# Optimization experiments

Hardware: AMD Instinct MI355X
Metric: run time of the kernel (lower is better)

Reference implementation:

```python
import jax, jax.numpy as jnp
import numpy as np

EPS = 1e-09

def setup_inputs() -> dict:
    key = jax.random.key(0)
    k1, k2, k3 = jax.random.split(key, 3)
    B, C, H, W = 16, 512, 64, 64
    K = 64  # node_num
    x = jax.random.normal(k1, (B, C, H, W), dtype=jnp.float32)
    anchor = jax.random.uniform(k2, (K, C), dtype=jnp.float32)
    sigma_raw = jax.random.uniform(k3, (K, C), dtype=jnp.float32)
    return {"x": x, "anchor": anchor, "sigma_raw": sigma_raw}

def _l2norm(v, axis):
    return v / jnp.maximum(jnp.linalg.norm(v, axis=axis, keepdims=True), 1e-12)

def reference(x, anchor, sigma_raw):
    B, C, H, W = x.shape
    K = anchor.shape[0]
    N = H * W
    sigma = jax.nn.sigmoid(sigma_raw)               # [K, C]
    xf = x.reshape(B, C, N).transpose(0, 2, 1)      # [B, N, C] descriptors

    # squared Mahalanobis-like distance ||(x - a_k)/s_k||^2 via expansion
    # (avoids materializing the [B, N, K, C] residual the torch loop builds)
    inv_s2 = 1.0 / (sigma * sigma)                  # [K, C]
    a_s2 = anchor * inv_s2                          # [K, C]
    const = jnp.sum(anchor * a_s2, axis=1)          # [K]
    d2 = (jnp.einsum('bnc,kc->bnk', xf * xf, inv_s2)
          - 2.0 * jnp.einsum('bnc,kc->bnk', xf, a_s2)
          + const[None, None, :])                   # [B, N, K]
    logits = (-0.5 * d2).transpose(0, 2, 1)         # [B, K, N]
    soft_assign = jax.nn.softmax(logits, axis=1)    # softmax over nodes

    # aggregation: nodes[b,k,c] = sum_n w * (x - a_k)/s_k / (sum_n w + eps)
    w_sum = jnp.sum(soft_assign, axis=2)            # [B, K]
    wx = jnp.einsum('bkn,bnc->bkc', soft_assign, xf)  # [B, K, C]
    nodes = (wx - w_sum[:, :, None] * anchor[None]) / sigma[None]
    nodes = nodes / (w_sum[:, :, None] + EPS)       # [B, K, C]

    nodes = _l2norm(nodes, axis=2)                  # intra-normalize per node
    flat = _l2norm(nodes.reshape(B, -1), axis=1)    # global L2
    # faithful to torch: flat [B, K*C] reinterpreted (no transpose) as [B, C, K]
    return flat.reshape(B, C, K), soft_assign
```

## Files before the change

### kernel.cpp

```cpp
#include <hip/hip_runtime.h>
#include <math.h>

#define B_ 16
#define C_ 512
#define N_ 4096
#define K_ 64

#define OFF_PBIG    0
#define OFF_INVSIG  131072
#define OFF_WSUM    163840
#define OFF_GSUM    164864
#define OFF_WX      164992

typedef short bf16x8 __attribute__((ext_vector_type(8)));
typedef float f32x16 __attribute__((ext_vector_type(16)));

union U4 { uint4 u; bf16x8 b; };

__device__ __forceinline__ unsigned hi16(float f) { return __float_as_uint(f) >> 16; }
__device__ __forceinline__ unsigned hi16rne(float f) {
  return (__float_as_uint(f) + 0x8000u) >> 16;
}
__device__ __forceinline__ float fromhi(unsigned h) { return __uint_as_float(h << 16); }
__device__ __forceinline__ unsigned pk(float lo, float hi) {
  return (__float_as_uint(lo) >> 16) | (__float_as_uint(hi) & 0xFFFF0000u);
}

__global__ void k_prep(const float* __restrict__ anchor,
                       const float* __restrict__ sraw,
                       unsigned* __restrict__ pbig,
                       float* __restrict__ invsig,
                       float* __restrict__ wsum,
                       float* __restrict__ gsum) {
  const int k = blockIdx.x;
  const int t = threadIdx.x;
  __shared__ float s_is2[C_], s_m[C_];
  __shared__ float red[4];
  float part = 0.f;
#pragma unroll
  for (int r = 0; r < 2; r++) {
    int c = r * 256 + t;
    float a = anchor[k * C_ + c];
    float sg = 1.f / (1.f + __expf(-sraw[k * C_ + c]));
    float is = 1.f / sg;
    float is2 = is * is;
    s_is2[c] = is2;
    s_m[c] = -2.f * a * is2;
    invsig[k * C_ + c] = is;
    part = fmaf(a * a, is2, part);
  }
  float v = part;
#pragma unroll
  for (int off = 32; off; off >>= 1) v += __shfl_down(v, off);
  if ((t & 63) == 0) red[t >> 6] = v;
  __syncthreads();
  float cst = red[0] + red[1] + red[2] + red[3];
  unsigned ch = hi16(cst);
  unsigned clr = hi16rne(cst - fromhi(ch));
#pragma unroll
  for (int r = 0; r < 2; r++) {
    int c = r * 256 + t;
    float is2 = s_is2[c], m = s_m[c];
    unsigned ih = hi16(is2);
    unsigned ilr = hi16rne(is2 - fromhi(ih));
    unsigned mh = hi16(m);
    unsigned mlr = hi16rne(m - fromhi(mh));
    unsigned* p = pbig + (size_t)k * 2048 + c * 4;
    p[0] = ih | (ilr << 16);
    p[1] = ih | (mh << 16);
    p[2] = mlr | (mh << 16);
    p[3] = (c == 0) ? (ch | (clr << 16)) : 0u;
  }
  if (k == 0) {
    for (int i = t; i < B_ * K_; i += 256) wsum[i] = 0.f;
    if (t < B_) gsum[t] = 0.f;
  }
}

__global__ __launch_bounds__(256) void k_dist(
    const float* __restrict__ x,
    const unsigned* __restrict__ pbig,
    float* __restrict__ soft,
    float* __restrict__ wsum) {
  const int b = blockIdx.y;
  const int nblk = blockIdx.x * 256;
  const int tid = threadIdx.x;
  const int wid = tid >> 6;
  const int lane = tid & 63;
  const int l31 = lane & 31;
  const int lh = lane >> 5;
  const int n0 = nblk + wid * 64;

  __shared__ unsigned ldsA[64 * 132];

  f32x16 acc[2][2];
#pragma unroll
  for (int kt = 0; kt < 2; kt++)
#pragma unroll
    for (int ns = 0; ns < 2; ns++)
#pragma unroll
      for (int i = 0; i < 16; i++) acc[kt][ns][i] = 0.f;

  const float* xb = x + (size_t)b * (C_ * N_);

  for (int chunk = 0; chunk < 16; chunk++) {
    const uint4* src = (const uint4*)pbig;
#pragma unroll
    for (int it = 0; it < 8; it++) {
      int flat = tid + it * 256;
      int k = flat >> 5, q = flat & 31;
      uint4 vv = src[(size_t)k * 512 + chunk * 32 + q];
      *(uint4*)&ldsA[k * 132 + q * 4] = vv;
    }
    __syncthreads();
    const int cchunk = chunk * 32;
    for (int kstep = 0; kstep < 16; kstep++) {
      U4 a0, a1;
      a0.u = *(const uint4*)&ldsA[l31 * 132 + kstep * 8 + lh * 4];
      a1.u = *(const uint4*)&ldsA[(32 + l31) * 132 + kstep * 8 + lh * 4];
      const int c = cchunk + kstep * 2 + lh;
      const float* xr = xb + (size_t)c * N_;
#pragma unroll
      for (int ns = 0; ns < 2; ns++) {
        float xv = xr[n0 + ns * 32 + l31];
        float x2 = xv * xv;
        unsigned u = __float_as_uint(xv);
        unsigned u2 = __float_as_uint(x2);
        unsigned uhf = u & 0xFFFF0000u;
        unsigned u2hf = u2 & 0xFFFF0000u;
        float xl = xv - __uint_as_float(uhf);
        float x2l = x2 - __uint_as_float(u2hf);
        U4 bf;
        bf.u.x = (u2 >> 16) | u2hf;
        bf.u.y = ((__float_as_uint(x2l) + 0x8000u) >> 16) | uhf;
        bf.u.z = (u >> 16) | ((__float_as_uint(xl) + 0x8000u) & 0xFFFF0000u);
        bf.u.w = (c == 0) ? 0x3F803F80u : 0u;
        acc[0][ns] = __builtin_amdgcn_mfma_f32_32x32x16_bf16(a0.b, bf.b, acc[0][ns], 0, 0, 0);
        acc[1][ns] = __builtin_amdgcn_mfma_f32_32x32x16_bf16(a1.b, bf.b, acc[1][ns], 0, 0, 0);
      }
    }
    __syncthreads();
  }

  float* softb = soft + (size_t)b * (K_ * N_);
#pragma unroll
  for (int ns = 0; ns < 2; ns++) {
    float mm = -3.4e38f;
#pragma unroll
    for (int kt = 0; kt < 2; kt++)
#pragma unroll
      for (int r = 0; r < 16; r++) {
        float l = -0.5f * acc[kt][ns][r];
        acc[kt][ns][r] = l;
        mm = fmaxf(mm, l);
      }
    mm = fmaxf(mm, __shfl_xor(mm, 32));
    float ss = 0.f;
#pragma unroll
    for (int kt = 0; kt < 2; kt++)
#pragma unroll
      for (int r = 0; r < 16; r++) {
        float e = __expf(acc[kt][ns][r] - mm);
        acc[kt][ns][r] = e;
        ss += e;
      }
    ss += __shfl_xor(ss, 32);
    float inv = 1.f / ss;
    const int nc = n0 + ns * 32 + l31;
#pragma unroll
    for (int kt = 0; kt < 2; kt++)
#pragma unroll
      for (int r = 0; r < 16; r++) {
        float w = acc[kt][ns][r] * inv;
        acc[kt][ns][r] = w;
        int k = kt * 32 + (r & 3) + 8 * (r >> 2) + 4 * lh;
        softb[(size_t)k * N_ + nc] = w;
      }
  }
#pragma unroll
  for (int kt = 0; kt < 2; kt++)
#pragma unroll
    for (int r = 0; r < 16; r++) {
      float v = acc[kt][0][r] + acc[kt][1][r];
      v += __shfl_xor(v, 1);
      v += __shfl_xor(v, 2);
      v += __shfl_xor(v, 4);
      v += __shfl_xor(v, 8);
      v += __shfl_xor(v, 16);
      if (l31 == 0) {
        int k = kt * 32 + (r & 3) + 8 * (r >> 2) + 4 * lh;
        atomicAdd(&wsum[b * K_ + k], v);
      }
    }
}

__global__ __launch_bounds__(256) void k_agg(const float* __restrict__ x,
                                             const float* __restrict__ soft,
                                             float* __restrict__ wx) {
  const int ct = blockIdx.x;
  const int b = blockIdx.y;
  const int tid = threadIdx.x;
  const int wid = tid >> 6, lane = tid & 63, l31 = lane & 31, lh = lane >> 5;
  const int c0 = ct * 32;
  const int n0 = wid * 1024;
  __shared__ float red[4][64][36];

  f32x16 acc[2];
#pragma unroll
  for (int kt = 0; kt < 2; kt++)
#pragma unroll
    for (int i = 0; i < 16; i++) acc[kt][i] = 0.f;

  const float* sb = soft + (size_t)b * (K_ * N_);
  const float* xr = x + (size_t)b * (C_ * N_) + (size_t)(c0 + l31) * N_;
  const float* s0 = sb + (size_t)l31 * N_;
  const float* s1 = sb + (size_t)(32 + l31) * N_;

  for (int kstep = 0; kstep < 64; kstep++) {
    int nb = n0 + kstep * 16 + lh * 8;
    float4 f0 = *(const float4*)&s0[nb];
    float4 f1 = *(const float4*)&s0[nb + 4];
    float4 g0 = *(const float4*)&s1[nb];
    float4 g1 = *(const float4*)&s1[nb + 4];
    float4 h0 = *(const float4*)&xr[nb];
    float4 h1 = *(const float4*)&xr[nb + 4];
    U4 A0, A1, Bf;
    A0.u.x = pk(f0.x, f0.y); A0.u.y = pk(f0.z, f0.w);
    A0.u.z = pk(f1.x, f1.y); A0.u.w = pk(f1.z, f1.w);
    A1.u.x = pk(g0.x, g0.y); A1.u.y = pk(g0.z, g0.w);
    A1.u.z = pk(g1.x, g1.y); A1.u.w = pk(g1.z, g1.w);
    Bf.u.x = pk(h0.x, h0.y); Bf.u.y = pk(h0.z, h0.w);
    Bf.u.z = pk(h1.x, h1.y); Bf.u.w = pk(h1.z, h1.w);
    acc[0] = __builtin_amdgcn_mfma_f32_32x32x16_bf16(A0.b, Bf.b, acc[0], 0, 0, 0);
    acc[1] = __builtin_amdgcn_mfma_f32_32x32x16_bf16(A1.b, Bf.b, acc[1], 0, 0, 0);
  }
#pragma unroll
  for (int kt = 0; kt < 2; kt++)
#pragma unroll
    for (int q = 0; q < 4; q++) {
      float4 vv = make_float4(acc[kt][q * 4], acc[kt][q * 4 + 1],
                              acc[kt][q * 4 + 2], acc[kt][q * 4 + 3]);
      *(float4*)&red[wid][lane][kt * 16 + q * 4] = vv;
    }
  __syncthreads();
  const int lt = tid & 63, sb4 = (tid >> 6) * 8;
  float v[8];
#pragma unroll
  for (int i = 0; i < 8; i++) v[i] = 0.f;
#pragma unroll
  for (int w = 0; w < 4; w++)
#pragma unroll
    for (int i = 0; i < 8; i++) v[i] += red[w][lt][sb4 + i];
#pragma unroll
  for (int i = 0; i < 8; i++) {
    int s = sb4 + i;
    int kt = s >> 4, r = s & 15;
    int k = kt * 32 + (r & 3) + 8 * (r >> 2) + 4 * (lt >> 5);
    wx[((size_t)b * K_ + k) * C_ + c0 + (lt & 31)] = v[i];
  }
}

__global__ void k_nodes(const float* __restrict__ wx,
                        const float* __restrict__ wsum,
                        const float* __restrict__ anchor,
                        const float* __restrict__ invsig,
                        float* __restrict__ out0,
                        float* __restrict__ gsum) {
  const int k = blockIdx.x, b = blockIdx.y;
  const int tid = threadIdx.x;
  float wsv = wsum[b * K_ + k];
  float winv = 1.f / (wsv + 1e-9f);
  float vals[4];
  float local = 0.f;
#pragma unroll
  for (int r = 0; r < 4; r++) {
    int c = r * 128 + tid;
    float w = wx[((size_t)b * K_ + k) * C_ + c];
    float v = (w - wsv * anchor[k * C_ + c]) * invsig[k * C_ + c] * winv;
    vals[r] = v;
    local = fmaf(v, v, local);
  }
  float v = local;
#pragma unroll
  for (int off = 32; off; off >>= 1) v += __shfl_down(v, off);
  __shared__ float red[2];
  if ((tid & 63) == 0) red[tid >> 6] = v;
  __syncthreads();
  float sumsq = red[0] + red[1];
  float norm = sqrtf(sumsq);
  float scale = 1.f / fmaxf(norm, 1e-12f);
#pragma unroll
  for (int r = 0; r < 4; r++) {
    int c = r * 128 + tid;
    out0[((size_t)b * K_ + k) * C_ + c] = vals[r] * scale;
  }
  if (tid == 0) atomicAdd(&gsum[b], sumsq * scale * scale);
}

__global__ void k_final(float* __restrict__ out0,
                        const float* __restrict__ gsum) {
  for (int i = blockIdx.x * 256 + threadIdx.x; i < B_ * K_ * C_;
       i += gridDim.x * 256) {
    int b = i >> 15;
    out0[i] = out0[i] * (1.f / fmaxf(sqrtf(gsum[b]), 1e-12f));
  }
}

extern "C" void kernel_launch(void* const* d_in, const int* in_sizes, int n_in,
                              void* d_out, int out_size, void* d_ws, size_t ws_size,
                              hipStream_t stream) {
  const float* x = (const float*)d_in[0];
  const float* anchor = (const float*)d_in[1];
  const float* sraw = (const float*)d_in[2];
  float* out0 = (float*)d_out;
  float* soft = out0 + (size_t)B_ * C_ * K_;
  float* ws = (float*)d_ws;

  unsigned* pbig = (unsigned*)(ws + OFF_PBIG);
  float* invsig = ws + OFF_INVSIG;
  float* wsum = ws + OFF_WSUM;
  float* gsum = ws + OFF_GSUM;
  float* wx = ws + OFF_WX;

  k_prep<<<K_, 256, 0, stream>>>(anchor, sraw, pbig, invsig, wsum, gsum);
  k_dist<<<dim3(N_ / 256, B_), 256, 0, stream>>>(x, pbig, soft, wsum);
  k_agg<<<dim3(C_ / 32, B_), 256, 0, stream>>>(x, soft, wx);
  k_nodes<<<dim3(K_, B_), 128, 0, stream>>>(wx, wsum, anchor, invsig, out0,
                                            gsum);
  k_final<<<512, 256, 0, stream>>>(out0, gsum);
}
```

Measured before the change: 303.4 us.

## Split channel reduction across waves in k_dist and N across blocks in k_agg

k_dist now processes 128 pixels per block, with wave pairs each reducing half of the channel dimension. Partial accumulators are exchanged through LDS and each wave finishes the softmax for 32 of the 64 nodes, using cross-wave max and sum reductions. k_agg splits the N reduction into two z-slices that write separate partial buffers, one of them reusing the output region as scratch, and k_nodes adds the two partials. Both changes double the grid size to raise occupancy and parallelism, at the cost of extra LDS traffic, more barriers and a larger shared-memory footprint.

```diff
diff --git a/kernel.cpp b/kernel.cpp
--- a/kernel.cpp
+++ b/kernel.cpp
@@ -83,15 +83,19 @@
     float* __restrict__ soft,
     float* __restrict__ wsum) {
   const int b = blockIdx.y;
-  const int nblk = blockIdx.x * 256;
+  const int nblk = blockIdx.x * 128;
   const int tid = threadIdx.x;
   const int wid = tid >> 6;
   const int lane = tid & 63;
   const int l31 = lane & 31;
   const int lh = lane >> 5;
-  const int n0 = nblk + wid * 64;
-
-  __shared__ unsigned ldsA[64 * 132];
+  const int chalf = wid & 1;
+  const int ktown = chalf;
+  const int n0 = nblk + (wid >> 1) * 64;
+
+  __shared__ unsigned ldsA[2 * 64 * 132];
+  __shared__ float cred[4][2][32];
+  __shared__ float csum[4][2][32];
 
   f32x16 acc[2][2];
 #pragma unroll
@@ -103,21 +107,25 @@
 
   const float* xb = x + (size_t)b * (C_ * N_);
 
-  for (int chunk = 0; chunk < 16; chunk++) {
+  for (int t = 0; t < 8; t++) {
     const uint4* src = (const uint4*)pbig;
 #pragma unroll
-    for (int it = 0; it < 8; it++) {
+    for (int it = 0; it < 16; it++) {
       int flat = tid + it * 256;
-      int k = flat >> 5, q = flat & 31;
-      uint4 vv = src[(size_t)k * 512 + chunk * 32 + q];
-      *(uint4*)&ldsA[k * 132 + q * 4] = vv;
+      int region = flat >> 11;
+      int within = flat & 2047;
+      int k = within >> 5, q = within & 31;
+      int ch = region * 8 + t;
+      uint4 vv = src[(size_t)k * 512 + ch * 32 + q];
+      *(uint4*)&ldsA[region * 8448 + k * 132 + q * 4] = vv;
     }
     __syncthreads();
-    const int cchunk = chunk * 32;
+    const unsigned* lbase = ldsA + chalf * 8448;
+    const int cchunk = (chalf * 8 + t) * 32;
     for (int kstep = 0; kstep < 16; kstep++) {
       U4 a0, a1;
-      a0.u = *(const uint4*)&ldsA[l31 * 132 + kstep * 8 + lh * 4];
-      a1.u = *(const uint4*)&ldsA[(32 + l31) * 132 + kstep * 8 + lh * 4];
+      a0.u = *(const uint4*)&lbase[l31 * 132 + kstep * 8 + lh * 4];
+      a1.u = *(const uint4*)&lbase[(32 + l31) * 132 + kstep * 8 + lh * 4];
       const int c = cchunk + kstep * 2 + lh;
       const float* xr = xb + (size_t)c * N_;
 #pragma unroll
@@ -142,67 +150,94 @@
     __syncthreads();
   }
 
+  float* exch = (float*)ldsA;
+  {
+    const int notown = 1 - ktown;
+#pragma unroll
+    for (int ns = 0; ns < 2; ns++)
+#pragma unroll
+      for (int q = 0; q < 4; q++) {
+        float4 vv = make_float4(acc[notown][ns][q * 4], acc[notown][ns][q * 4 + 1],
+                                acc[notown][ns][q * 4 + 2], acc[notown][ns][q * 4 + 3]);
+        *(float4*)&exch[((wid * 64 + lane) * 36) + ns * 16 + q * 4] = vv;
+      }
+  }
+  __syncthreads();
+  {
+    const float* pex = &exch[(((wid ^ 1) * 64 + lane) * 36)];
+#pragma unroll
+    for (int ns = 0; ns < 2; ns++)
+#pragma unroll
+      for (int r = 0; r < 16; r++) acc[ktown][ns][r] += pex[ns * 16 + r];
+  }
+
   float* softb = soft + (size_t)b * (K_ * N_);
 #pragma unroll
   for (int ns = 0; ns < 2; ns++) {
-    float mm = -3.4e38f;
-#pragma unroll
-    for (int kt = 0; kt < 2; kt++)
-#pragma unroll
-      for (int r = 0; r < 16; r++) {
-        float l = -0.5f * acc[kt][ns][r];
-        acc[kt][ns][r] = l;
-        mm = fmaxf(mm, l);
-      }
-    mm = fmaxf(mm, __shfl_xor(mm, 32));
+    float m = -3.4e38f;
+#pragma unroll
+    for (int r = 0; r < 16; r++) {
+      float l = -0.5f * acc[ktown][ns][r];
+      acc[ktown][ns][r] = l;
+      m = fmaxf(m, l);
+    }
+    m = fmaxf(m, __shfl_xor(m, 32));
+    if (lh == 0) cred[wid][ns][l31] = m;
+  }
+  __syncthreads();
+#pragma unroll
+  for (int ns = 0; ns < 2; ns++) {
+    float m = fmaxf(cred[wid][ns][l31], cred[wid ^ 1][ns][l31]);
     float ss = 0.f;
 #pragma unroll
-    for (int kt = 0; kt < 2; kt++)
-#pragma unroll
-      for (int r = 0; r < 16; r++) {
-        float e = __expf(acc[kt][ns][r] - mm);
-        acc[kt][ns][r] = e;
-        ss += e;
-      }
+    for (int r = 0; r < 16; r++) {
+      float e = __expf(acc[ktown][ns][r] - m);
+      acc[ktown][ns][r] = e;
+      ss += e;
+    }
     ss += __shfl_xor(ss, 32);
-    float inv = 1.f / ss;
+    if (lh == 0) csum[wid][ns][l31] = ss;
+  }
+  __syncthreads();
+#pragma unroll
+  for (int ns = 0; ns < 2; ns++) {
+    float tot = csum[wid][ns][l31] + csum[wid ^ 1][ns][l31];
+    float iv = 1.f / tot;
     const int nc = n0 + ns * 32 + l31;
 #pragma unroll
-    for (int kt = 0; kt < 2; kt++)
-#pragma unroll
-      for (int r = 0; r < 16; r++) {
-        float w = acc[kt][ns][r] * inv;
-        acc[kt][ns][r] = w;
-        int k = kt * 32 + (r & 3) + 8 * (r >> 2) + 4 * lh;
-        softb[(size_t)k * N_ + nc] = w;
-      }
-  }
-#pragma unroll
-  for (int kt = 0; kt < 2; kt++)
-#pragma unroll
     for (int r = 0; r < 16; r++) {
-      float v = acc[kt][0][r] + acc[kt][1][r];
-      v += __shfl_xor(v, 1);
-      v += __shfl_xor(v, 2);
-      v += __shfl_xor(v, 4);
-      v += __shfl_xor(v, 8);
-      v += __shfl_xor(v, 16);
-      if (l31 == 0) {
-        int k = kt * 32 + (r & 3) + 8 * (r >> 2) + 4 * lh;
-        atomicAdd(&wsum[b * K_ + k], v);
-      }
-    }
+      float w = acc[ktown][ns][r] * iv;
+      acc[ktown][ns][r] = w;
+      int k = ktown * 32 + (r & 3) + 8 * (r >> 2) + 4 * lh;
+      softb[(size_t)k * N_ + nc] = w;
+    }
+  }
+#pragma unroll
+  for (int r = 0; r < 16; r++) {
+    float v = acc[ktown][0][r] + acc[ktown][1][r];
+    v += __shfl_xor(v, 1);
+    v += __shfl_xor(v, 2);
+    v += __shfl_xor(v, 4);
+    v += __shfl_xor(v, 8);
+    v += __shfl_xor(v, 16);
+    if (l31 == 0) {
+      int k = ktown * 32 + (r & 3) + 8 * (r >> 2) + 4 * lh;
+      atomicAdd(&wsum[b * K_ + k], v);
+    }
+  }
 }
 
 __global__ __launch_bounds__(256) void k_agg(const float* __restrict__ x,
                                              const float* __restrict__ soft,
-                                             float* __restrict__ wx) {
+                                             float* __restrict__ wxp0,
+                                             float* __restrict__ wxp1) {
   const int ct = blockIdx.x;
   const int b = blockIdx.y;
+  const int z = blockIdx.z;
   const int tid = threadIdx.x;
   const int wid = tid >> 6, lane = tid & 63, l31 = lane & 31, lh = lane >> 5;
   const int c0 = ct * 32;
-  const int n0 = wid * 1024;
+  const int n0 = z * 2048 + wid * 512;
   __shared__ float red[4][64][36];
 
   f32x16 acc[2];
@@ -216,7 +251,7 @@
   const float* s0 = sb + (size_t)l31 * N_;
   const float* s1 = sb + (size_t)(32 + l31) * N_;
 
-  for (int kstep = 0; kstep < 64; kstep++) {
+  for (int kstep = 0; kstep < 32; kstep++) {
     int nb = n0 + kstep * 16 + lh * 8;
     float4 f0 = *(const float4*)&s0[nb];
     float4 f1 = *(const float4*)&s0[nb + 4];
@@ -243,6 +278,7 @@
       *(float4*)&red[wid][lane][kt * 16 + q * 4] = vv;
     }
   __syncthreads();
+  float* wxp = z ? wxp1 : wxp0;
   const int lt = tid & 63, sb4 = (tid >> 6) * 8;
   float v[8];
 #pragma unroll
@@ -256,11 +292,12 @@
     int s = sb4 + i;
     int kt = s >> 4, r = s & 15;
     int k = kt * 32 + (r & 3) + 8 * (r >> 2) + 4 * (lt >> 5);
-    wx[((size_t)b * K_ + k) * C_ + c0 + (lt & 31)] = v[i];
-  }
-}
-
-__global__ void k_nodes(const float* __restrict__ wx,
+    wxp[((size_t)b * K_ + k) * C_ + c0 + (lt & 31)] = v[i];
+  }
+}
+
+__global__ void k_nodes(const float* __restrict__ wxp0,
+                        const float* __restrict__ wxp1,
                         const float* __restrict__ wsum,
                         const float* __restrict__ anchor,
                         const float* __restrict__ invsig,
@@ -275,7 +312,8 @@
 #pragma unroll
   for (int r = 0; r < 4; r++) {
     int c = r * 128 + tid;
-    float w = wx[((size_t)b * K_ + k) * C_ + c];
+    size_t idx = ((size_t)b * K_ + k) * C_ + c;
+    float w = wxp0[idx] + wxp1[idx];
     float v = (w - wsv * anchor[k * C_ + c]) * invsig[k * C_ + c] * winv;
     vals[r] = v;
     local = fmaf(v, v, local);
@@ -320,12 +358,13 @@
   float* invsig = ws + OFF_INVSIG;
   float* wsum = ws + OFF_WSUM;
   float* gsum = ws + OFF_GSUM;
-  float* wx = ws + OFF_WX;
+  float* wx1 = ws + OFF_WX;
+  float* wx0 = out0;
 
   k_prep<<<K_, 256, 0, stream>>>(anchor, sraw, pbig, invsig, wsum, gsum);
-  k_dist<<<dim3(N_ / 256, B_), 256, 0, stream>>>(x, pbig, soft, wsum);
-  k_agg<<<dim3(C_ / 32, B_), 256, 0, stream>>>(x, soft, wx);
-  k_nodes<<<dim3(K_, B_), 128, 0, stream>>>(wx, wsum, anchor, invsig, out0,
-                                            gsum);
+  k_dist<<<dim3(N_ / 128, B_), 256, 0, stream>>>(x, pbig, soft, wsum);
+  k_agg<<<dim3(C_ / 32, B_, 2), 256, 0, stream>>>(x, soft, wx0, wx1);
+  k_nodes<<<dim3(K_, B_), 128, 0, stream>>>(wx0, wx1, wsum, anchor, invsig,
+                                            out0, gsum);
   k_final<<<512, 256, 0, stream>>>(out0, gsum);
 }
```

Measured after the change: 405.1 us. 1.34x slower.

## Double block counts in distance and aggregation kernels with split-N partial sums

Applied to the files above, without the earlier changes.

k_dist now gives each wave 32 columns instead of 64, doubling the grid to 512 blocks with a swizzled block-to-(batch, n-tile) mapping. Each chunk's 16 x values are prefetched into registers before the LDS fill. k_agg splits the N reduction into two halves along a z grid dimension, writing partials to out0 and to workspace, which k_nodes then sums. The aim is to fill more CUs and hide latency better; the cost is twice as many redundant anchor-tile loads per output, more wsum atomics, and an extra partial buffer read.

```diff
diff --git a/kernel.cpp b/kernel.cpp
--- a/kernel.cpp
+++ b/kernel.cpp
@@ -82,28 +82,31 @@
     const unsigned* __restrict__ pbig,
     float* __restrict__ soft,
     float* __restrict__ wsum) {
-  const int b = blockIdx.y;
-  const int nblk = blockIdx.x * 256;
+  const int bid = blockIdx.x;
+  const int swz = (bid & 7) * 64 + (bid >> 3);
+  const int b = swz >> 5;
+  const int nblk = (swz & 31) * 128;
   const int tid = threadIdx.x;
   const int wid = tid >> 6;
   const int lane = tid & 63;
   const int l31 = lane & 31;
   const int lh = lane >> 5;
-  const int n0 = nblk + wid * 64;
+  const int n0 = nblk + wid * 32;
 
   __shared__ unsigned ldsA[64 * 132];
 
-  f32x16 acc[2][2];
-#pragma unroll
-  for (int kt = 0; kt < 2; kt++)
-#pragma unroll
-    for (int ns = 0; ns < 2; ns++)
-#pragma unroll
-      for (int i = 0; i < 16; i++) acc[kt][ns][i] = 0.f;
+  f32x16 acc0, acc1;
+#pragma unroll
+  for (int i = 0; i < 16; i++) { acc0[i] = 0.f; acc1[i] = 0.f; }
 
   const float* xb = x + (size_t)b * (C_ * N_);
+  const float* xcol = xb + n0 + l31;
 
   for (int chunk = 0; chunk < 16; chunk++) {
+    float xreg[16];
+#pragma unroll
+    for (int kk = 0; kk < 16; kk++)
+      xreg[kk] = xcol[(size_t)(chunk * 32 + kk * 2 + lh) * N_];
     const uint4* src = (const uint4*)pbig;
 #pragma unroll
     for (int it = 0; it < 8; it++) {
@@ -113,96 +116,89 @@
       *(uint4*)&ldsA[k * 132 + q * 4] = vv;
     }
     __syncthreads();
-    const int cchunk = chunk * 32;
+#pragma unroll
     for (int kstep = 0; kstep < 16; kstep++) {
       U4 a0, a1;
       a0.u = *(const uint4*)&ldsA[l31 * 132 + kstep * 8 + lh * 4];
       a1.u = *(const uint4*)&ldsA[(32 + l31) * 132 + kstep * 8 + lh * 4];
-      const int c = cchunk + kstep * 2 + lh;
-      const float* xr = xb + (size_t)c * N_;
-#pragma unroll
-      for (int ns = 0; ns < 2; ns++) {
-        float xv = xr[n0 + ns * 32 + l31];
-        float x2 = xv * xv;
-        unsigned u = __float_as_uint(xv);
-        unsigned u2 = __float_as_uint(x2);
-        unsigned uhf = u & 0xFFFF0000u;
-        unsigned u2hf = u2 & 0xFFFF0000u;
-        float xl = xv - __uint_as_float(uhf);
-        float x2l = x2 - __uint_as_float(u2hf);
-        U4 bf;
-        bf.u.x = (u2 >> 16) | u2hf;
-        bf.u.y = ((__float_as_uint(x2l) + 0x8000u) >> 16) | uhf;
-        bf.u.z = (u >> 16) | ((__float_as_uint(xl) + 0x8000u) & 0xFFFF0000u);
-        bf.u.w = (c == 0) ? 0x3F803F80u : 0u;
-        acc[0][ns] = __builtin_amdgcn_mfma_f32_32x32x16_bf16(a0.b, bf.b, acc[0][ns], 0, 0, 0);
-        acc[1][ns] = __builtin_amdgcn_mfma_f32_32x32x16_bf16(a1.b, bf.b, acc[1][ns], 0, 0, 0);
-      }
+      const int c = chunk * 32 + kstep * 2 + lh;
+      float xv = xreg[kstep];
+      float x2 = xv * xv;
+      unsigned u = __float_as_uint(xv);
+      unsigned u2 = __float_as_uint(x2);
+      unsigned uhf = u & 0xFFFF0000u;
+      unsigned u2hf = u2 & 0xFFFF0000u;
+      float xl = xv - __uint_as_float(uhf);
+      float x2l = x2 - __uint_as_float(u2hf);
+      U4 bf;
+      bf.u.x = (u2 >> 16) | u2hf;
+      bf.u.y = ((__float_as_uint(x2l) + 0x8000u) >> 16) | uhf;
+      bf.u.z = (u >> 16) | ((__float_as_uint(xl) + 0x8000u) & 0xFFFF0000u);
+      bf.u.w = (c == 0) ? 0x3F803F80u : 0u;
+      acc0 = __builtin_amdgcn_mfma_f32_32x32x16_bf16(a0.b, bf.b, acc0, 0, 0, 0);
+      acc1 = __builtin_amdgcn_mfma_f32_32x32x16_bf16(a1.b, bf.b, acc1, 0, 0, 0);
     }
     __syncthreads();
   }
 
   float* softb = soft + (size_t)b * (K_ * N_);
-#pragma unroll
-  for (int ns = 0; ns < 2; ns++) {
-    float mm = -3.4e38f;
-#pragma unroll
-    for (int kt = 0; kt < 2; kt++)
-#pragma unroll
-      for (int r = 0; r < 16; r++) {
-        float l = -0.5f * acc[kt][ns][r];
-        acc[kt][ns][r] = l;
-        mm = fmaxf(mm, l);
-      }
-    mm = fmaxf(mm, __shfl_xor(mm, 32));
-    float ss = 0.f;
-#pragma unroll
-    for (int kt = 0; kt < 2; kt++)
-#pragma unroll
-      for (int r = 0; r < 16; r++) {
-        float e = __expf(acc[kt][ns][r] - mm);
-        acc[kt][ns][r] = e;
-        ss += e;
-      }
-    ss += __shfl_xor(ss, 32);
-    float inv = 1.f / ss;
-    const int nc = n0 + ns * 32 + l31;
-#pragma unroll
-    for (int kt = 0; kt < 2; kt++)
-#pragma unroll
-      for (int r = 0; r < 16; r++) {
-        float w = acc[kt][ns][r] * inv;
-        acc[kt][ns][r] = w;
-        int k = kt * 32 + (r & 3) + 8 * (r >> 2) + 4 * lh;
-        softb[(size_t)k * N_ + nc] = w;
-      }
-  }
-#pragma unroll
-  for (int kt = 0; kt < 2; kt++)
-#pragma unroll
-    for (int r = 0; r < 16; r++) {
-      float v = acc[kt][0][r] + acc[kt][1][r];
-      v += __shfl_xor(v, 1);
-      v += __shfl_xor(v, 2);
-      v += __shfl_xor(v, 4);
-      v += __shfl_xor(v, 8);
-      v += __shfl_xor(v, 16);
-      if (l31 == 0) {
-        int k = kt * 32 + (r & 3) + 8 * (r >> 2) + 4 * lh;
-        atomicAdd(&wsum[b * K_ + k], v);
-      }
+  float mm = -3.4e38f;
+#pragma unroll
+  for (int r = 0; r < 16; r++) {
+    acc0[r] *= -0.5f; mm = fmaxf(mm, acc0[r]);
+    acc1[r] *= -0.5f; mm = fmaxf(mm, acc1[r]);
+  }
+  mm = fmaxf(mm, __shfl_xor(mm, 32));
+  float ss = 0.f;
+#pragma unroll
+  for (int r = 0; r < 16; r++) {
+    acc0[r] = __expf(acc0[r] - mm); ss += acc0[r];
+    acc1[r] = __expf(acc1[r] - mm); ss += acc1[r];
+  }
+  ss += __shfl_xor(ss, 32);
+  float inv = 1.f / ss;
+  const int nc = n0 + l31;
+#pragma unroll
+  for (int r = 0; r < 16; r++) {
+    int k0 = (r & 3) + 8 * (r >> 2) + 4 * lh;
+    float w0 = acc0[r] * inv; acc0[r] = w0;
+    softb[(size_t)k0 * N_ + nc] = w0;
+    float w1 = acc1[r] * inv; acc1[r] = w1;
+    softb[(size_t)(32 + k0) * N_ + nc] = w1;
+  }
+#pragma unroll
+  for (int r = 0; r < 16; r++) {
+    float v0 = acc0[r];
+    v0 += __shfl_xor(v0, 1);
+    v0 += __shfl_xor(v0, 2);
+    v0 += __shfl_xor(v0, 4);
+    v0 += __shfl_xor(v0, 8);
+    v0 += __shfl_xor(v0, 16);
+    float v1 = acc1[r];
+    v1 += __shfl_xor(v1, 1);
+    v1 += __shfl_xor(v1, 2);
+    v1 += __shfl_xor(v1, 4);
+    v1 += __shfl_xor(v1, 8);
+    v1 += __shfl_xor(v1, 16);
+    if (l31 == 0) {
+      int k0 = (r & 3) + 8 * (r >> 2) + 4 * lh;
+      atomicAdd(&wsum[b * K_ + k0], v0);
+      atomicAdd(&wsum[b * K_ + 32 + k0], v1);
     }
+  }
 }
 
 __global__ __launch_bounds__(256) void k_agg(const float* __restrict__ x,
                                              const float* __restrict__ soft,
-                                             float* __restrict__ wx) {
+                                             float* __restrict__ wxp0,
+                                             float* __restrict__ wxp1) {
   const int ct = blockIdx.x;
   const int b = blockIdx.y;
+  const int z = blockIdx.z;
   const int tid = threadIdx.x;
   const int wid = tid >> 6, lane = tid & 63, l31 = lane & 31, lh = lane >> 5;
   const int c0 = ct * 32;
-  const int n0 = wid * 1024;
+  const int n0 = z * 2048 + wid * 512;
   __shared__ float red[4][64][36];
 
   f32x16 acc[2];
@@ -216,7 +212,7 @@
   const float* s0 = sb + (size_t)l31 * N_;
   const float* s1 = sb + (size_t)(32 + l31) * N_;
 
-  for (int kstep = 0; kstep < 64; kstep++) {
+  for (int kstep = 0; kstep < 32; kstep++) {
     int nb = n0 + kstep * 16 + lh * 8;
     float4 f0 = *(const float4*)&s0[nb];
     float4 f1 = *(const float4*)&s0[nb + 4];
@@ -243,6 +239,7 @@
       *(float4*)&red[wid][lane][kt * 16 + q * 4] = vv;
     }
   __syncthreads();
+  float* wxp = z ? wxp1 : wxp0;
   const int lt = tid & 63, sb4 = (tid >> 6) * 8;
   float v[8];
 #pragma unroll
@@ -256,11 +253,12 @@
     int s = sb4 + i;
     int kt = s >> 4, r = s & 15;
     int k = kt * 32 + (r & 3) + 8 * (r >> 2) + 4 * (lt >> 5);
-    wx[((size_t)b * K_ + k) * C_ + c0 + (lt & 31)] = v[i];
-  }
-}
-
-__global__ void k_nodes(const float* __restrict__ wx,
+    wxp[((size_t)b * K_ + k) * C_ + c0 + (lt & 31)] = v[i];
+  }
+}
+
+__global__ void k_nodes(const float* __restrict__ wxp0,
+                        const float* __restrict__ wxp1,
                         const float* __restrict__ wsum,
                         const float* __restrict__ anchor,
                         const float* __restrict__ invsig,
@@ -275,7 +273,8 @@
 #pragma unroll
   for (int r = 0; r < 4; r++) {
     int c = r * 128 + tid;
-    float w = wx[((size_t)b * K_ + k) * C_ + c];
+    size_t idx = ((size_t)b * K_ + k) * C_ + c;
+    float w = wxp0[idx] + wxp1[idx];
     float v = (w - wsv * anchor[k * C_ + c]) * invsig[k * C_ + c] * winv;
     vals[r] = v;
     local = fmaf(v, v, local);
@@ -320,12 +319,13 @@
   float* invsig = ws + OFF_INVSIG;
   float* wsum = ws + OFF_WSUM;
   float* gsum = ws + OFF_GSUM;
-  float* wx = ws + OFF_WX;
+  float* wx1 = ws + OFF_WX;
+  float* wx0 = out0;
 
   k_prep<<<K_, 256, 0, stream>>>(anchor, sraw, pbig, invsig, wsum, gsum);
-  k_dist<<<dim3(N_ / 256, B_), 256, 0, stream>>>(x, pbig, soft, wsum);
-  k_agg<<<dim3(C_ / 32, B_), 256, 0, stream>>>(x, soft, wx);
-  k_nodes<<<dim3(K_, B_), 128, 0, stream>>>(wx, wsum, anchor, invsig, out0,
-                                            gsum);
+  k_dist<<<512, 256, 0, stream>>>(x, pbig, soft, wsum);
+  k_agg<<<dim3(C_ / 32, B_, 2), 256, 0, stream>>>(x, soft, wx0, wx1);
+  k_nodes<<<dim3(K_, B_), 128, 0, stream>>>(wx0, wx1, wsum, anchor, invsig,
+                                            out0, gsum);
   k_final<<<512, 256, 0, stream>>>(out0, gsum);
 }
```

New measurement: 349.3 us. +15.1%, slower.

## Restructure distance and aggregation kernels for more blocks, XCD swizzle, and LDS-free A loads

Applied to the files above, without the earlier changes.

k_prep now writes the packed anchor/sigma operand in MFMA fragment order so k_dist can load A fragments straight from global memory without LDS staging or barriers. k_dist splits the 64 nodes across wave pairs, which shrinks the accumulators and lets the grid grow to 1024 XCD-swizzled blocks. It double-buffers the x column loads in registers, and the cross-wave softmax now goes through a small shared-memory max/sum exchange. k_agg splits N into four slices across 1024 swizzled blocks and accumulates into a zeroed wx with atomics, trading extra atomic traffic for more parallelism and occupancy.

```diff
diff --git a/kernel.cpp b/kernel.cpp
--- a/kernel.cpp
+++ b/kernel.cpp
@@ -31,7 +31,8 @@
                        unsigned* __restrict__ pbig,
                        float* __restrict__ invsig,
                        float* __restrict__ wsum,
-                       float* __restrict__ gsum) {
+                       float* __restrict__ gsum,
+                       float* __restrict__ wx) {
   const int k = blockIdx.x;
   const int t = threadIdx.x;
   __shared__ float s_is2[C_], s_m[C_];
@@ -65,144 +66,161 @@
     unsigned ilr = hi16rne(is2 - fromhi(ih));
     unsigned mh = hi16(m);
     unsigned mlr = hi16rne(m - fromhi(mh));
-    unsigned* p = pbig + (size_t)k * 2048 + c * 4;
-    p[0] = ih | (ilr << 16);
-    p[1] = ih | (mh << 16);
-    p[2] = mlr | (mh << 16);
-    p[3] = (c == 0) ? (ch | (clr << 16)) : 0u;
-  }
+    int chunk = c >> 5, ks = (c & 31) >> 1, lh = c & 1;
+    int kh = k >> 5;
+    size_t dst = ((((size_t)chunk * 16 + ks) * 2 + kh) * 64 + lh * 32 + (k & 31)) * 4;
+    pbig[dst + 0] = ih | (ilr << 16);
+    pbig[dst + 1] = ih | (mh << 16);
+    pbig[dst + 2] = mlr | (mh << 16);
+    pbig[dst + 3] = (c == 0) ? (ch | (clr << 16)) : 0u;
+  }
+  float4 z4 = make_float4(0.f, 0.f, 0.f, 0.f);
+  float4* wz = (float4*)(wx + (size_t)k * 8192);
+#pragma unroll
+  for (int it = 0; it < 8; it++) wz[it * 256 + t] = z4;
   if (k == 0) {
     for (int i = t; i < B_ * K_; i += 256) wsum[i] = 0.f;
     if (t < B_) gsum[t] = 0.f;
   }
 }
 
-__global__ __launch_bounds__(256) void k_dist(
+__global__ __launch_bounds__(256, 4) void k_dist(
     const float* __restrict__ x,
     const unsigned* __restrict__ pbig,
     float* __restrict__ soft,
     float* __restrict__ wsum) {
-  const int b = blockIdx.y;
-  const int nblk = blockIdx.x * 256;
+  const int bid = blockIdx.x;
+  const int swz = (bid & 7) * 128 + (bid >> 3);
+  const int b = swz >> 6;
+  const int nblk = (swz & 63) * 64;
   const int tid = threadIdx.x;
   const int wid = tid >> 6;
   const int lane = tid & 63;
   const int l31 = lane & 31;
   const int lh = lane >> 5;
-  const int n0 = nblk + wid * 64;
-
-  __shared__ unsigned ldsA[64 * 132];
-
-  f32x16 acc[2][2];
-#pragma unroll
-  for (int kt = 0; kt < 2; kt++)
-#pragma unroll
-    for (int ns = 0; ns < 2; ns++)
-#pragma unroll
-      for (int i = 0; i < 16; i++) acc[kt][ns][i] = 0.f;
-
-  const float* xb = x + (size_t)b * (C_ * N_);
-
-  for (int chunk = 0; chunk < 16; chunk++) {
-    const uint4* src = (const uint4*)pbig;
-#pragma unroll
-    for (int it = 0; it < 8; it++) {
-      int flat = tid + it * 256;
-      int k = flat >> 5, q = flat & 31;
-      uint4 vv = src[(size_t)k * 512 + chunk * 32 + q];
-      *(uint4*)&ldsA[k * 132 + q * 4] = vv;
-    }
-    __syncthreads();
-    const int cchunk = chunk * 32;
-    for (int kstep = 0; kstep < 16; kstep++) {
-      U4 a0, a1;
-      a0.u = *(const uint4*)&ldsA[l31 * 132 + kstep * 8 + lh * 4];
-      a1.u = *(const uint4*)&ldsA[(32 + l31) * 132 + kstep * 8 + lh * 4];
-      const int c = cchunk + kstep * 2 + lh;
-      const float* xr = xb + (size_t)c * N_;
-#pragma unroll
-      for (int ns = 0; ns < 2; ns++) {
-        float xv = xr[n0 + ns * 32 + l31];
-        float x2 = xv * xv;
-        unsigned u = __float_as_uint(xv);
-        unsigned u2 = __float_as_uint(x2);
-        unsigned uhf = u & 0xFFFF0000u;
-        unsigned u2hf = u2 & 0xFFFF0000u;
-        float xl = xv - __uint_as_float(uhf);
-        float x2l = x2 - __uint_as_float(u2hf);
-        U4 bf;
-        bf.u.x = (u2 >> 16) | u2hf;
-        bf.u.y = ((__float_as_uint(x2l) + 0x8000u) >> 16) | uhf;
-        bf.u.z = (u >> 16) | ((__float_as_uint(xl) + 0x8000u) & 0xFFFF0000u);
-        bf.u.w = (c == 0) ? 0x3F803F80u : 0u;
-        acc[0][ns] = __builtin_amdgcn_mfma_f32_32x32x16_bf16(a0.b, bf.b, acc[0][ns], 0, 0, 0);
-        acc[1][ns] = __builtin_amdgcn_mfma_f32_32x32x16_bf16(a1.b, bf.b, acc[1][ns], 0, 0, 0);
+  const int kh = wid & 1;
+  const int n0 = nblk + (wid >> 1) * 32;
+
+  __shared__ float cmax[4][32];
+  __shared__ float csum[4][32];
+
+  f32x16 acc;
+#pragma unroll
+  for (int i = 0; i < 16; i++) acc[i] = 0.f;
+
+  const float* xcol = x + (size_t)b * (C_ * N_) + n0 + l31;
+  const uint4* pf = (const uint4*)pbig + (size_t)kh * 64 + lane;
+
+  float xa[16], xb_[16];
+#pragma unroll
+  for (int kk = 0; kk < 16; kk++)
+    xa[kk] = xcol[(size_t)(kk * 2 + lh) * N_];
+
+#define PACKMF(XV, CC, ACC, AFRAG)                                            \
+  {                                                                           \
+    float xv = (XV);                                                          \
+    float x2 = xv * xv;                                                       \
+    unsigned u = __float_as_uint(xv);                                         \
+    unsigned u2 = __float_as_uint(x2);                                        \
+    unsigned uhf = u & 0xFFFF0000u;                                           \
+    unsigned u2hf = u2 & 0xFFFF0000u;                                         \
+    float xl = xv - __uint_as_float(uhf);                                     \
+    float x2l = x2 - __uint_as_float(u2hf);                                   \
+    U4 bf;                                                                    \
+    bf.u.x = (u2 >> 16) | u2hf;                                               \
+    bf.u.y = ((__float_as_uint(x2l) + 0x8000u) >> 16) | uhf;                  \
+    bf.u.z = (u >> 16) | ((__float_as_uint(xl) + 0x8000u) & 0xFFFF0000u);     \
+    bf.u.w = ((CC) == 0) ? 0x3F803F80u : 0u;                                  \
+    ACC = __builtin_amdgcn_mfma_f32_32x32x16_bf16((AFRAG), bf.b, ACC, 0, 0, 0); \
+  }
+
+  for (int c2 = 0; c2 < 8; c2++) {
+    {
+      const int chunk = 2 * c2;
+#pragma unroll
+      for (int kk = 0; kk < 16; kk++)
+        xb_[kk] = xcol[(size_t)((chunk + 1) * 32 + kk * 2 + lh) * N_];
+#pragma unroll
+      for (int ks = 0; ks < 16; ks++) {
+        U4 a;
+        a.u = pf[(size_t)(chunk * 16 + ks) * 128];
+        PACKMF(xa[ks], chunk * 32 + ks * 2 + lh, acc, a.b);
       }
     }
-    __syncthreads();
-  }
-
-  float* softb = soft + (size_t)b * (K_ * N_);
-#pragma unroll
-  for (int ns = 0; ns < 2; ns++) {
-    float mm = -3.4e38f;
-#pragma unroll
-    for (int kt = 0; kt < 2; kt++)
-#pragma unroll
-      for (int r = 0; r < 16; r++) {
-        float l = -0.5f * acc[kt][ns][r];
-        acc[kt][ns][r] = l;
-        mm = fmaxf(mm, l);
+    {
+      const int chunk = 2 * c2 + 1;
+      if (c2 < 7) {
+#pragma unroll
+        for (int kk = 0; kk < 16; kk++)
+          xa[kk] = xcol[(size_t)((chunk + 1) * 32 + kk * 2 + lh) * N_];
       }
-    mm = fmaxf(mm, __shfl_xor(mm, 32));
-    float ss = 0.f;
-#pragma unroll
-    for (int kt = 0; kt < 2; kt++)
-#pragma unroll
-      for (int r = 0; r < 16; r++) {
-        float e = __expf(acc[kt][ns][r] - mm);
-        acc[kt][ns][r] = e;
-        ss += e;
-      }
-    ss += __shfl_xor(ss, 32);
-    float inv = 1.f / ss;
-    const int nc = n0 + ns * 32 + l31;
-#pragma unroll
-    for (int kt = 0; kt < 2; kt++)
-#pragma unroll
-      for (int r = 0; r < 16; r++) {
-        float w = acc[kt][ns][r] * inv;
-        acc[kt][ns][r] = w;
-        int k = kt * 32 + (r & 3) + 8 * (r >> 2) + 4 * lh;
-        softb[(size_t)k * N_ + nc] = w;
-      }
-  }
-#pragma unroll
-  for (int kt = 0; kt < 2; kt++)
-#pragma unroll
-    for (int r = 0; r < 16; r++) {
-      float v = acc[kt][0][r] + acc[kt][1][r];
-      v += __shfl_xor(v, 1);
-      v += __shfl_xor(v, 2);
-      v += __shfl_xor(v, 4);
-      v += __shfl_xor(v, 8);
-      v += __shfl_xor(v, 16);
-      if (l31 == 0) {
-        int k = kt * 32 + (r & 3) + 8 * (r >> 2) + 4 * lh;
-        atomicAdd(&wsum[b * K_ + k], v);
+#pragma unroll
+      for (int ks = 0; ks < 16; ks++) {
+        U4 a;
+        a.u = pf[(size_t)(chunk * 16 + ks) * 128];
+        PACKMF(xb_[ks], chunk * 32 + ks * 2 + lh, acc, a.b);
       }
     }
-}
-
-__global__ __launch_bounds__(256) void k_agg(const float* __restrict__ x,
-                                             const float* __restrict__ soft,
-                                             float* __restrict__ wx) {
-  const int ct = blockIdx.x;
-  const int b = blockIdx.y;
+  }
+#undef PACKMF
+
+  float* softb = soft + (size_t)b * (K_ * N_);
+  float mm = -3.4e38f;
+#pragma unroll
+  for (int r = 0; r < 16; r++) {
+    acc[r] *= -0.5f;
+    mm = fmaxf(mm, acc[r]);
+  }
+  mm = fmaxf(mm, __shfl_xor(mm, 32));
+  cmax[wid][l31] = mm;
+  __syncthreads();
+  float m = fmaxf(cmax[wid][l31], cmax[wid ^ 1][l31]);
+  float ss = 0.f;
+#pragma unroll
+  for (int r = 0; r < 16; r++) {
+    acc[r] = __expf(acc[r] - m);
+    ss += acc[r];
+  }
+  ss += __shfl_xor(ss, 32);
+  csum[wid][l31] = ss;
+  __syncthreads();
+  float tot = csum[wid][l31] + csum[wid ^ 1][l31];
+  float inv = 1.f / tot;
+  const int nc = n0 + l31;
+#pragma unroll
+  for (int r = 0; r < 16; r++) {
+    float w = acc[r] * inv;
+    acc[r] = w;
+    int k0 = kh * 32 + (r & 3) + 8 * (r >> 2) + 4 * lh;
+    softb[(size_t)k0 * N_ + nc] = w;
+  }
+#pragma unroll
+  for (int r = 0; r < 16; r++) {
+    float v = acc[r];
+    v += __shfl_xor(v, 1);
+    v += __shfl_xor(v, 2);
+    v += __shfl_xor(v, 4);
+    v += __shfl_xor(v, 8);
+    v += __shfl_xor(v, 16);
+    if (l31 == 0) {
+      int k0 = kh * 32 + (r & 3) + 8 * (r >> 2) + 4 * lh;
+      atomicAdd(&wsum[b * K_ + k0], v);
+    }
+  }
+}
+
+__global__ __launch_bounds__(256, 4) void k_agg(const float* __restrict__ x,
+                                                const float* __restrict__ soft,
+                                                float* __restrict__ wx) {
+  const int bid = blockIdx.x;
+  const int xcd = bid & 7, slot = bid >> 3;
+  const int grp = (slot >> 4) * 8 + xcd;
+  const int ct = slot & 15;
+  const int b = grp & 15, z = grp >> 4;
   const int tid = threadIdx.x;
   const int wid = tid >> 6, lane = tid & 63, l31 = lane & 31, lh = lane >> 5;
   const int c0 = ct * 32;
-  const int n0 = wid * 1024;
+  const int n0 = z * 1024 + wid * 256;
   __shared__ float red[4][64][36];
 
   f32x16 acc[2];
@@ -216,7 +234,7 @@
   const float* s0 = sb + (size_t)l31 * N_;
   const float* s1 = sb + (size_t)(32 + l31) * N_;
 
-  for (int kstep = 0; kstep < 64; kstep++) {
+  for (int kstep = 0; kstep < 16; kstep++) {
     int nb = n0 + kstep * 16 + lh * 8;
     float4 f0 = *(const float4*)&s0[nb];
     float4 f1 = *(const float4*)&s0[nb + 4];
@@ -256,7 +274,7 @@
     int s = sb4 + i;
     int kt = s >> 4, r = s & 15;
     int k = kt * 32 + (r & 3) + 8 * (r >> 2) + 4 * (lt >> 5);
-    wx[((size_t)b * K_ + k) * C_ + c0 + (lt & 31)] = v[i];
+    atomicAdd(&wx[((size_t)b * K_ + k) * C_ + c0 + (lt & 31)], v[i]);
   }
 }
 
@@ -322,9 +340,9 @@
   float* gsum = ws + OFF_GSUM;
   float* wx = ws + OFF_WX;
 
-  k_prep<<<K_, 256, 0, stream>>>(anchor, sraw, pbig, invsig, wsum, gsum);
-  k_dist<<<dim3(N_ / 256, B_), 256, 0, stream>>>(x, pbig, soft, wsum);
-  k_agg<<<dim3(C_ / 32, B_), 256, 0, stream>>>(x, soft, wx);
+  k_prep<<<K_, 256, 0, stream>>>(anchor, sraw, pbig, invsig, wsum, gsum, wx);
+  k_dist<<<1024, 256, 0, stream>>>(x, pbig, soft, wsum);
+  k_agg<<<1024, 256, 0, stream>>>(x, soft, wx);
   k_nodes<<<dim3(K_, B_), 128, 0, stream>>>(wx, wsum, anchor, invsig, out0,
                                             gsum);
   k_final<<<512, 256, 0, stream>>>(out0, gsum);
```

Measured after the change: 328.6 us. +8.3%, slower.
